# Kernel optimization log

Measured on AMD Instinct MI355X. Metric: run time of the kernel, lower is better.

Reference implementation:

```python
import jax, jax.numpy as jnp
import numpy as np

EMBED_DIM = 1024
NUM_HEADS = 16
HEAD_DIM = EMBED_DIM // NUM_HEADS
SCALE = HEAD_DIM ** -0.5


def setup_inputs() -> dict:
    key = jax.random.key(0)
    ks = jax.random.split(key, 9)
    B, N = 2, 2048
    s = EMBED_DIM ** -0.5  # ~ torch Linear init scale
    x = jax.random.normal(ks[0], (B, N, EMBED_DIM), dtype=jnp.float32)
    Wq = jax.random.uniform(ks[1], (EMBED_DIM, EMBED_DIM), jnp.float32, -s, s)
    bq = jax.random.uniform(ks[2], (EMBED_DIM,), jnp.float32, -s, s)
    Wk = jax.random.uniform(ks[3], (EMBED_DIM, EMBED_DIM), jnp.float32, -s, s)
    bk = jax.random.uniform(ks[4], (EMBED_DIM,), jnp.float32, -s, s)
    Wv = jax.random.uniform(ks[5], (EMBED_DIM, EMBED_DIM), jnp.float32, -s, s)
    bv = jax.random.uniform(ks[6], (EMBED_DIM,), jnp.float32, -s, s)
    Wo = jax.random.uniform(ks[7], (EMBED_DIM, EMBED_DIM), jnp.float32, -s, s)
    bo = jax.random.uniform(ks[8], (EMBED_DIM,), jnp.float32, -s, s)
    return {"x": x, "Wq": Wq, "bq": bq, "Wk": Wk, "bk": bk,
            "Wv": Wv, "bv": bv, "Wo": Wo, "bo": bo}


def reference(x, Wq, bq, Wk, bk, Wv, bv, Wo, bo):
    B, N, R = x.shape
    H, D = NUM_HEADS, HEAD_DIM
    # projections: Linear(x) = x @ W^T + b; reshape to (B, H, N, D)
    def proj(W, b):
        return (x @ W.T + b).reshape(B, N, H, D).transpose(0, 2, 1, 3)
    q = proj(Wq, bq)
    k = proj(Wk, bk)
    v = proj(Wv, bv)
    attn = jnp.einsum('bhnd,bhmd->bhnm', q, k) * SCALE  # (B,H,N,N)
    attn = jax.nn.softmax(attn, axis=-1)
    out = jnp.einsum('bhnm,bhmd->bhnd', attn, v)        # (B,H,N,D)
    out = out.transpose(0, 2, 1, 3).reshape(B, N, R)
    return out @ Wo.T + bo
```

## Files before the change

### kernel.cpp

```cpp
#include <hip/hip_runtime.h>
#include <stdint.h>

typedef __bf16 bf16;
typedef __bf16 bf16x4 __attribute__((ext_vector_type(4)));
typedef __bf16 bf16x8 __attribute__((ext_vector_type(8)));
typedef float f32x4 __attribute__((ext_vector_type(4)));

#define MFMA16(a, b, c) __builtin_amdgcn_mfma_f32_16x16x32_bf16((a), (b), (c), 0, 0, 0)

#define EMBED 1024
#define SEQ   2048
#define MROWS 4096
#define ATTN_SCALE 0.125f

__device__ __forceinline__ void gl2lds16(const bf16* g, bf16* l) {
    __builtin_amdgcn_global_load_lds(
        (const __attribute__((address_space(1))) void*)g,
        (__attribute__((address_space(3))) void*)l,
        16, 0, 0);
}

__global__ __launch_bounds__(256) void cast_all_kernel(
    const float* __restrict__ x,  const float* __restrict__ Wq,
    const float* __restrict__ Wk, const float* __restrict__ Wv,
    const float* __restrict__ Wo, bf16* __restrict__ dst) {
    const int blk = blockIdx.x;
    const float* src;
    size_t so, dofs;
    if (blk < 2048) {
        src = x; so = (size_t)blk * 2048; dofs = so;
    } else {
        const int w = (blk - 2048) >> 9;
        so  = (size_t)((blk - 2048) & 511) * 2048;
        src = (w == 0) ? Wq : (w == 1) ? Wk : (w == 2) ? Wv : Wo;
        dofs = (size_t)(4 + w) * 1024 * 1024 + so;
    }
    const size_t i = (size_t)threadIdx.x * 8;
    float4 a = *(const float4*)(src + so + i);
    float4 b = *(const float4*)(src + so + i + 4);
    bf16x8 o;
    o[0] = (bf16)a.x; o[1] = (bf16)a.y; o[2] = (bf16)a.z; o[3] = (bf16)a.w;
    o[4] = (bf16)b.x; o[5] = (bf16)b.y; o[6] = (bf16)b.z; o[7] = (bf16)b.w;
    *(bf16x8*)(dst + dofs + i) = o;
}

template <bool SCALE>
__device__ __forceinline__ void gemm_tile(const bf16* __restrict__ A,
                                          const bf16* __restrict__ W,
                                          const float* __restrict__ bias,
                                          bf16* __restrict__ C,
                                          int m0, int n0, bf16* smem) {
    bf16* As = smem;
    bf16* Bs = smem + 128 * 64;

    const int lane = threadIdx.x & 63;
    const int wv   = threadIdx.x >> 6;
    const int wm   = (wv >> 1) * 64;
    const int wn   = (wv & 1) * 64;
    const int fr   = lane & 15;
    const int quad = lane >> 4;
    const int srow = wv * 8 + (lane >> 3);
    const int swz  = (((lane & 7) ^ ((lane >> 3) & 7))) * 8;

    f32x4 acc[4][4];
#pragma unroll
    for (int mt = 0; mt < 4; ++mt)
#pragma unroll
        for (int nt = 0; nt < 4; ++nt)
            acc[mt][nt] = (f32x4){0.f, 0.f, 0.f, 0.f};

    for (int k0 = 0; k0 < 1024; k0 += 64) {
#pragma unroll
        for (int i = 0; i < 4; ++i) {
            gl2lds16(A + (size_t)(m0 + i * 32 + srow) * 1024 + k0 + swz,
                     &As[(i * 32 + wv * 8) * 64]);
            gl2lds16(W + (size_t)(n0 + i * 32 + srow) * 1024 + k0 + swz,
                     &Bs[(i * 32 + wv * 8) * 64]);
        }
        __syncthreads();
#pragma unroll
        for (int ks = 0; ks < 2; ++ks) {
            const int fcol = ((ks * 4 + quad) ^ (fr & 7)) * 8;
            bf16x8 af[4], bfr[4];
#pragma unroll
            for (int t = 0; t < 4; ++t) {
                af[t]  = *(const bf16x8*)&As[(wm + t * 16 + fr) * 64 + fcol];
                bfr[t] = *(const bf16x8*)&Bs[(wn + t * 16 + fr) * 64 + fcol];
            }
#pragma unroll
            for (int mt = 0; mt < 4; ++mt)
#pragma unroll
                for (int nt = 0; nt < 4; ++nt)
                    acc[mt][nt] = MFMA16(af[mt], bfr[nt], acc[mt][nt]);
        }
        __syncthreads();
    }

    float bv[4];
#pragma unroll
    for (int nt = 0; nt < 4; ++nt)
        bv[nt] = bias[n0 + wn + nt * 16 + fr];
    const int row4 = quad * 4;
#pragma unroll
    for (int mt = 0; mt < 4; ++mt)
#pragma unroll
        for (int nt = 0; nt < 4; ++nt)
#pragma unroll
            for (int r = 0; r < 4; ++r) {
                int m = m0 + wm + mt * 16 + row4 + r;
                int n = n0 + wn + nt * 16 + fr;
                float v = acc[mt][nt][r] + bv[nt];
                if (SCALE) v *= ATTN_SCALE;
                C[(size_t)m * 1024 + n] = (bf16)v;
            }
}

__device__ __forceinline__ void v_tile(const bf16* __restrict__ x,
                                       const bf16* __restrict__ Wv,
                                       const float* __restrict__ bias,
                                       bf16* __restrict__ VT,
                                       int m0, int n0, bf16* smem) {
    bf16* As = smem;
    bf16* Bs = smem + 128 * 64;

    const int lane = threadIdx.x & 63;
    const int wv   = threadIdx.x >> 6;
    const int wmW  = (wv >> 1) * 64;
    const int wnT  = (wv & 1) * 64;
    const int f    = lane & 15;
    const int quad = lane >> 4;
    const int srow = wv * 8 + (lane >> 3);
    const int swz  = (((lane & 7) ^ ((lane >> 3) & 7))) * 8;

    f32x4 acc[4][4];
#pragma unroll
    for (int mt = 0; mt < 4; ++mt)
#pragma unroll
        for (int nt = 0; nt < 4; ++nt)
            acc[mt][nt] = (f32x4){0.f, 0.f, 0.f, 0.f};

    for (int k0 = 0; k0 < 1024; k0 += 64) {
#pragma unroll
        for (int i = 0; i < 4; ++i) {
            gl2lds16(x  + (size_t)(m0 + i * 32 + srow) * 1024 + k0 + swz,
                     &As[(i * 32 + wv * 8) * 64]);
            gl2lds16(Wv + (size_t)(n0 + i * 32 + srow) * 1024 + k0 + swz,
                     &Bs[(i * 32 + wv * 8) * 64]);
        }
        __syncthreads();
#pragma unroll
        for (int ks = 0; ks < 2; ++ks) {
            const int fcol = ((ks * 4 + quad) ^ (f & 7)) * 8;
            bf16x8 wf[4], xf[4];
#pragma unroll
            for (int t = 0; t < 4; ++t) {
                wf[t] = *(const bf16x8*)&Bs[(wmW + t * 16 + f) * 64 + fcol];
                xf[t] = *(const bf16x8*)&As[(wnT + t * 16 + f) * 64 + fcol];
            }
#pragma unroll
            for (int mt = 0; mt < 4; ++mt)
#pragma unroll
                for (int nt = 0; nt < 4; ++nt)
                    acc[mt][nt] = MFMA16(wf[mt], xf[nt], acc[mt][nt]);
        }
        __syncthreads();
    }

    float4 b4[4];
#pragma unroll
    for (int mt = 0; mt < 4; ++mt)
        b4[mt] = *(const float4*)&bias[n0 + wmW + mt * 16 + quad * 4];

#pragma unroll
    for (int mt = 0; mt < 4; ++mt)
#pragma unroll
        for (int nt = 0; nt < 4; ++nt) {
            const int tok = wnT + nt * 16 + f;
#pragma unroll
            for (int r = 0; r < 4; ++r) {
                const float bvr = (r == 0) ? b4[mt].x : (r == 1) ? b4[mt].y
                                : (r == 2) ? b4[mt].z : b4[mt].w;
                smem[(wmW + mt * 16 + quad * 4 + r) * 136 + tok] =
                    (bf16)(acc[mt][nt][r] + bvr);
            }
        }
    __syncthreads();

    const int n_r  = threadIdx.x >> 4;
    const int t8   = (threadIdx.x & 15) * 8;
    const int base = t8 & ~31;
    const int u4   = ((t8 >> 3) & 3) * 4;
    const int bb   = m0 >> 11;
    const int tokg = (m0 & 2047) + t8;
#pragma unroll
    for (int p = 0; p < 8; ++p) {
        const int n_loc = p * 16 + n_r;
        const bf16* row = &smem[n_loc * 136];
        bf16x4 a = *(const bf16x4*)&row[base + u4];
        bf16x4 b = *(const bf16x4*)&row[base + 16 + u4];
        bf16x8 v = {a[0], a[1], a[2], a[3], b[0], b[1], b[2], b[3]};
        *(bf16x8*)&VT[((size_t)(bb * 1024 + n0 + n_loc)) * 2048 + tokg] = v;
    }
}

__global__ __launch_bounds__(256) void qkv_kernel(
    const bf16* __restrict__ x,
    const bf16* __restrict__ Wq, const float* __restrict__ bq,
    const bf16* __restrict__ Wk, const float* __restrict__ bk,
    const bf16* __restrict__ Wv, const float* __restrict__ bv,
    bf16* __restrict__ Q, bf16* __restrict__ K, bf16* __restrict__ VT) {
    __shared__ __align__(16) bf16 smem[128 * 136];
    const int m0    = blockIdx.x * 128;
    const int which = blockIdx.y >> 3;
    const int n0    = (blockIdx.y & 7) * 128;
    if (which == 0)      gemm_tile<true>(x, Wq, bq, Q, m0, n0, smem);
    else if (which == 1) gemm_tile<false>(x, Wk, bk, K, m0, n0, smem);
    else                 v_tile(x, Wv, bv, VT, m0, n0, smem);
}

__global__ __launch_bounds__(256) void oproj_kernel(
    const bf16* __restrict__ A, const bf16* __restrict__ W,
    const float* __restrict__ bias, float* __restrict__ C) {
    const int m0 = blockIdx.x * 128;
    const int n0 = blockIdx.y * 64;

    __shared__ bf16 As[128 * 64];
    __shared__ bf16 Bs[64 * 64];

    const int lane = threadIdx.x & 63;
    const int wv   = threadIdx.x >> 6;
    const int wm   = (wv >> 1) * 64;
    const int wn   = (wv & 1) * 32;
    const int fr   = lane & 15;
    const int quad = lane >> 4;
    const int srow = wv * 8 + (lane >> 3);
    const int swz  = (((lane & 7) ^ ((lane >> 3) & 7))) * 8;

    f32x4 acc[4][2];
#pragma unroll
    for (int mt = 0; mt < 4; ++mt)
#pragma unroll
        for (int nt = 0; nt < 2; ++nt)
            acc[mt][nt] = (f32x4){0.f, 0.f, 0.f, 0.f};

    for (int k0 = 0; k0 < 1024; k0 += 64) {
#pragma unroll
        for (int i = 0; i < 4; ++i)
            gl2lds16(A + (size_t)(m0 + i * 32 + srow) * 1024 + k0 + swz,
                     &As[(i * 32 + wv * 8) * 64]);
#pragma unroll
        for (int i = 0; i < 2; ++i)
            gl2lds16(W + (size_t)(n0 + i * 32 + srow) * 1024 + k0 + swz,
                     &Bs[(i * 32 + wv * 8) * 64]);
        __syncthreads();
#pragma unroll
        for (int ks = 0; ks < 2; ++ks) {
            const int fcol = ((ks * 4 + quad) ^ (fr & 7)) * 8;
            bf16x8 af[4], bfr[2];
#pragma unroll
            for (int t = 0; t < 4; ++t)
                af[t] = *(const bf16x8*)&As[(wm + t * 16 + fr) * 64 + fcol];
#pragma unroll
            for (int t = 0; t < 2; ++t)
                bfr[t] = *(const bf16x8*)&Bs[(wn + t * 16 + fr) * 64 + fcol];
#pragma unroll
            for (int mt = 0; mt < 4; ++mt)
#pragma unroll
                for (int nt = 0; nt < 2; ++nt)
                    acc[mt][nt] = MFMA16(af[mt], bfr[nt], acc[mt][nt]);
        }
        __syncthreads();
    }

    float bv[2];
#pragma unroll
    for (int nt = 0; nt < 2; ++nt)
        bv[nt] = bias[n0 + wn + nt * 16 + fr];
    const int row4 = quad * 4;
#pragma unroll
    for (int mt = 0; mt < 4; ++mt)
#pragma unroll
        for (int nt = 0; nt < 2; ++nt)
#pragma unroll
            for (int r = 0; r < 4; ++r) {
                int m = m0 + wm + mt * 16 + row4 + r;
                int n = n0 + wn + nt * 16 + fr;
                C[(size_t)m * 1024 + n] = acc[mt][nt][r] + bv[nt];
            }
}

__global__ __launch_bounds__(256, 2) void attn_kernel(
    const bf16* __restrict__ Q, const bf16* __restrict__ K,
    const bf16* __restrict__ VT, bf16* __restrict__ Opart,
    float* __restrict__ lpart) {
    const int tid  = threadIdx.x;
    const int lane = tid & 63;
    const int wv   = tid >> 6;
    const int quad = lane >> 4;
    const int f    = lane & 15;
    const int qt   = blockIdx.x >> 1;
    const int half = blockIdx.x & 1;
    const int q0   = qt * 256;
    const int kvb  = half * 1024;
    const int b    = blockIdx.y >> 4;
    const int h    = blockIdx.y & 15;

    const bf16* Qp = Q + ((size_t)b * SEQ) * 1024 + (size_t)h * 64;
    const bf16* Kp = K + ((size_t)b * SEQ) * 1024 + (size_t)h * 64;
    const bf16* Vp = VT + ((size_t)(b * 1024 + h * 64)) * 2048;
    bf16*  Op = Opart + (size_t)half * MROWS * 1024
                      + ((size_t)b * SEQ) * 1024 + (size_t)h * 64;
    float* lp = lpart + ((size_t)(half * 2 + b) * 16 + h) * SEQ;

    __shared__ bf16 Ks[2][64 * 64];
    __shared__ bf16 VTs[2][64 * 64];

    bf16x8 qf[4][2];
#pragma unroll
    for (int qg = 0; qg < 4; ++qg) {
        const bf16* qrow = Qp + (size_t)(q0 + wv * 64 + qg * 16 + f) * 1024;
        qf[qg][0] = *(const bf16x8*)(qrow + quad * 8);
        qf[qg][1] = *(const bf16x8*)(qrow + 32 + quad * 8);
    }

    const int srow = wv * 8 + (lane >> 3);
    const int swz  = (((lane & 7) ^ ((lane >> 3) & 7))) * 8;
    auto stageK = [&](int kv0, int buf) {
#pragma unroll
        for (int i = 0; i < 2; ++i)
            gl2lds16(Kp + (size_t)(kv0 + i * 32 + srow) * 1024 + swz,
                     &Ks[buf][(i * 32 + wv * 8) * 64]);
    };
    auto stageVT = [&](int kv0, int buf) {
#pragma unroll
        for (int i = 0; i < 2; ++i)
            gl2lds16(Vp + (size_t)(i * 32 + srow) * 2048 + kv0 + swz,
                     &VTs[buf][(i * 32 + wv * 8) * 64]);
    };

    stageK(kvb, 0);
    stageVT(kvb, 0);

    f32x4 oacc[4][4];
#pragma unroll
    for (int qg = 0; qg < 4; ++qg)
#pragma unroll
        for (int t = 0; t < 4; ++t)
            oacc[qg][t] = (f32x4){0.f, 0.f, 0.f, 0.f};
    f32x4 lacc[4];
#pragma unroll
    for (int qg = 0; qg < 4; ++qg)
        lacc[qg] = (f32x4){0.f, 0.f, 0.f, 0.f};
    const bf16x8 ones8 = {(bf16)1.f, (bf16)1.f, (bf16)1.f, (bf16)1.f,
                          (bf16)1.f, (bf16)1.f, (bf16)1.f, (bf16)1.f};
    const f32x4  zero4 = (f32x4){0.f, 0.f, 0.f, 0.f};

    const int fcol0 = (quad ^ (f & 7)) * 8;
    const int fcol1 = ((4 + quad) ^ (f & 7)) * 8;

    __syncthreads();

    auto step = [&](int cur, int nextit) {
        if (nextit < 16) {
            stageK(kvb + nextit * 64, cur ^ 1);
            stageVT(kvb + nextit * 64, cur ^ 1);
        }

        bf16x8 kf0[4], kf1[4];
#pragma unroll
        for (int t = 0; t < 4; ++t) {
            kf0[t] = *(const bf16x8*)&Ks[cur][(t * 16 + f) * 64 + fcol0];
            kf1[t] = *(const bf16x8*)&Ks[cur][(t * 16 + f) * 64 + fcol1];
        }
        bf16x8 pb8[4][2];
#pragma unroll
        for (int qg = 0; qg < 4; ++qg) {
            f32x4 s[4];
#pragma unroll
            for (int t = 0; t < 4; ++t) {
                s[t] = MFMA16(kf0[t], qf[qg][0], zero4);
                s[t] = MFMA16(kf1[t], qf[qg][1], s[t]);
            }
#pragma unroll
            for (int kt = 0; kt < 2; ++kt) {
#pragma unroll
                for (int r = 0; r < 4; ++r) {
                    pb8[qg][kt][r]     = (bf16)__expf(s[2 * kt][r]);
                    pb8[qg][kt][4 + r] = (bf16)__expf(s[2 * kt + 1][r]);
                }
                lacc[qg] = MFMA16(ones8, pb8[qg][kt], lacc[qg]);
            }
        }

#pragma unroll
        for (int dt = 0; dt < 4; ++dt) {
#pragma unroll
            for (int kt = 0; kt < 2; ++kt) {
                const int pc = ((kt * 4 + quad) ^ (f & 7)) * 8;
                bf16x8 vf = *(const bf16x8*)&VTs[cur][(dt * 16 + f) * 64 + pc];
#pragma unroll
                for (int qg = 0; qg < 4; ++qg)
                    oacc[qg][dt] = MFMA16(vf, pb8[qg][kt], oacc[qg][dt]);
            }
        }
        __syncthreads();
    };

    for (int it = 0; it < 16; it += 2) {
        step(0, it + 1);
        step(1, it + 2);
    }

#pragma unroll
    for (int qg = 0; qg < 4; ++qg) {
        const int q = q0 + wv * 64 + qg * 16 + f;
        bf16* orow = Op + (size_t)q * 1024;
#pragma unroll
        for (int dt = 0; dt < 4; ++dt) {
            bf16x4 ov;
#pragma unroll
            for (int r = 0; r < 4; ++r)
                ov[r] = (bf16)oacc[qg][dt][r];
            *(bf16x4*)(orow + dt * 16 + quad * 4) = ov;
        }
        if (quad == 0)
            lp[q] = lacc[qg][0];
    }
}

__global__ __launch_bounds__(256) void combine_kernel(
    const bf16* __restrict__ Opart, const float* __restrict__ lpart,
    bf16* __restrict__ O) {
    const int gid = blockIdx.x * 256 + threadIdx.x;
    const int row = gid >> 7;
    const int c8  = (gid & 127) * 8;
    const int b   = row >> 11;
    const int tok = row & 2047;
    const int h   = c8 >> 6;

    const float l = lpart[((size_t)(0 * 2 + b) * 16 + h) * SEQ + tok]
                  + lpart[((size_t)(1 * 2 + b) * 16 + h) * SEQ + tok];
    const float inv = 1.0f / l;

    const size_t off = (size_t)row * 1024 + c8;
    bf16x8 a = *(const bf16x8*)&Opart[off];
    bf16x8 c = *(const bf16x8*)&Opart[(size_t)MROWS * 1024 + off];
    bf16x8 o;
#pragma unroll
    for (int i = 0; i < 8; ++i)
        o[i] = (bf16)(((float)a[i] + (float)c[i]) * inv);
    *(bf16x8*)&O[off] = o;
}

extern "C" void kernel_launch(void* const* d_in, const int* in_sizes, int n_in,
                              void* d_out, int out_size, void* d_ws, size_t ws_size,
                              hipStream_t stream) {
    const float* x  = (const float*)d_in[0];
    const float* Wq = (const float*)d_in[1];
    const float* bq = (const float*)d_in[2];
    const float* Wk = (const float*)d_in[3];
    const float* bk = (const float*)d_in[4];
    const float* Wv = (const float*)d_in[5];
    const float* bv = (const float*)d_in[6];
    const float* Wo = (const float*)d_in[7];
    const float* bo = (const float*)d_in[8];
    float* out = (float*)d_out;

    bf16* xb    = (bf16*)d_ws;
    bf16* Wqb   = xb   + (size_t)MROWS * 1024;
    bf16* Wkb   = Wqb  + (size_t)1024 * 1024;
    bf16* Wvb   = Wkb  + (size_t)1024 * 1024;
    bf16* Wob   = Wvb  + (size_t)1024 * 1024;
    bf16* Q     = Wob  + (size_t)1024 * 1024;
    bf16* K     = Q    + (size_t)MROWS * 1024;
    bf16* VT    = K    + (size_t)MROWS * 1024;
    bf16* O     = VT   + (size_t)MROWS * 1024;
    bf16* Opart = O    + (size_t)MROWS * 1024;
    float* lpart = (float*)(Opart + (size_t)2 * MROWS * 1024);

    cast_all_kernel<<<4096, 256, 0, stream>>>(x, Wq, Wk, Wv, Wo, xb);

    qkv_kernel<<<dim3(32, 24), 256, 0, stream>>>(xb, Wqb, bq, Wkb, bk, Wvb, bv, Q, K, VT);
    attn_kernel<<<dim3(16, 32), 256, 0, stream>>>(Q, K, VT, Opart, lpart);
    combine_kernel<<<2048, 256, 0, stream>>>(Opart, lpart, O);
    oproj_kernel<<<dim3(32, 16), 256, 0, stream>>>(O, Wob, bo, out);
}
```

Measured before the change: 193.6 us.

## Double-buffer GEMM tiles, deepen attention K/V prefetch, use exp2 with folded scale

The three GEMM paths (QKV projection, V-transpose tile, output projection) now stage the next K-tile into a second LDS buffer while computing the current one, with one barrier per iteration instead of two. The attention kernel moves from a 2-buffer to a 4-buffer ring with prefetch distance 2 and partial vmcnt waits, so loads stay in flight across barriers. The softmax exponent now uses native exp2, with log2(e) folded into the Q scale constant. MFMA sections are wrapped in s_setprio to favour matrix issue. LDS use roughly doubles, which may reduce occupancy.

```diff
diff --git a/kernel.cpp b/kernel.cpp
--- a/kernel.cpp
+++ b/kernel.cpp
@@ -11,7 +11,7 @@
 #define EMBED 1024
 #define SEQ   2048
 #define MROWS 4096
-#define ATTN_SCALE 0.125f
+#define ATTN_QSCALE 0.1803368801111f
 
 __device__ __forceinline__ void gl2lds16(const bf16* g, bf16* l) {
     __builtin_amdgcn_global_load_lds(
@@ -50,9 +50,6 @@
                                           const float* __restrict__ bias,
                                           bf16* __restrict__ C,
                                           int m0, int n0, bf16* smem) {
-    bf16* As = smem;
-    bf16* Bs = smem + 128 * 64;
-
     const int lane = threadIdx.x & 63;
     const int wv   = threadIdx.x >> 6;
     const int wm   = (wv >> 1) * 64;
@@ -69,7 +66,10 @@
         for (int nt = 0; nt < 4; ++nt)
             acc[mt][nt] = (f32x4){0.f, 0.f, 0.f, 0.f};
 
-    for (int k0 = 0; k0 < 1024; k0 += 64) {
+    auto stage = [&](int kt, int bb) {
+        bf16* As = smem + bb * 16384;
+        bf16* Bs = As + 8192;
+        const int k0 = kt * 64;
 #pragma unroll
         for (int i = 0; i < 4; ++i) {
             gl2lds16(A + (size_t)(m0 + i * 32 + srow) * 1024 + k0 + swz,
@@ -77,7 +77,17 @@
             gl2lds16(W + (size_t)(n0 + i * 32 + srow) * 1024 + k0 + swz,
                      &Bs[(i * 32 + wv * 8) * 64]);
         }
-        __syncthreads();
+    };
+
+    stage(0, 0);
+#pragma unroll
+    for (int kt = 0; kt < 16; ++kt) {
+        const int bb = kt & 1;
+        asm volatile("s_waitcnt vmcnt(0)" ::: "memory");
+        __builtin_amdgcn_s_barrier();
+        if (kt < 15) stage(kt + 1, bb ^ 1);
+        const bf16* As = smem + bb * 16384;
+        const bf16* Bs = As + 8192;
 #pragma unroll
         for (int ks = 0; ks < 2; ++ks) {
             const int fcol = ((ks * 4 + quad) ^ (fr & 7)) * 8;
@@ -87,13 +97,14 @@
                 af[t]  = *(const bf16x8*)&As[(wm + t * 16 + fr) * 64 + fcol];
                 bfr[t] = *(const bf16x8*)&Bs[(wn + t * 16 + fr) * 64 + fcol];
             }
+            __builtin_amdgcn_s_setprio(1);
 #pragma unroll
             for (int mt = 0; mt < 4; ++mt)
 #pragma unroll
                 for (int nt = 0; nt < 4; ++nt)
                     acc[mt][nt] = MFMA16(af[mt], bfr[nt], acc[mt][nt]);
-        }
-        __syncthreads();
+            __builtin_amdgcn_s_setprio(0);
+        }
     }
 
     float bv[4];
@@ -110,7 +121,7 @@
                 int m = m0 + wm + mt * 16 + row4 + r;
                 int n = n0 + wn + nt * 16 + fr;
                 float v = acc[mt][nt][r] + bv[nt];
-                if (SCALE) v *= ATTN_SCALE;
+                if (SCALE) v *= ATTN_QSCALE;
                 C[(size_t)m * 1024 + n] = (bf16)v;
             }
 }
@@ -120,9 +131,6 @@
                                        const float* __restrict__ bias,
                                        bf16* __restrict__ VT,
                                        int m0, int n0, bf16* smem) {
-    bf16* As = smem;
-    bf16* Bs = smem + 128 * 64;
-
     const int lane = threadIdx.x & 63;
     const int wv   = threadIdx.x >> 6;
     const int wmW  = (wv >> 1) * 64;
@@ -139,7 +147,10 @@
         for (int nt = 0; nt < 4; ++nt)
             acc[mt][nt] = (f32x4){0.f, 0.f, 0.f, 0.f};
 
-    for (int k0 = 0; k0 < 1024; k0 += 64) {
+    auto stage = [&](int kt, int bb) {
+        bf16* As = smem + bb * 16384;
+        bf16* Bs = As + 8192;
+        const int k0 = kt * 64;
 #pragma unroll
         for (int i = 0; i < 4; ++i) {
             gl2lds16(x  + (size_t)(m0 + i * 32 + srow) * 1024 + k0 + swz,
@@ -147,7 +158,17 @@
             gl2lds16(Wv + (size_t)(n0 + i * 32 + srow) * 1024 + k0 + swz,
                      &Bs[(i * 32 + wv * 8) * 64]);
         }
-        __syncthreads();
+    };
+
+    stage(0, 0);
+#pragma unroll
+    for (int kt = 0; kt < 16; ++kt) {
+        const int bb = kt & 1;
+        asm volatile("s_waitcnt vmcnt(0)" ::: "memory");
+        __builtin_amdgcn_s_barrier();
+        if (kt < 15) stage(kt + 1, bb ^ 1);
+        const bf16* As = smem + bb * 16384;
+        const bf16* Bs = As + 8192;
 #pragma unroll
         for (int ks = 0; ks < 2; ++ks) {
             const int fcol = ((ks * 4 + quad) ^ (f & 7)) * 8;
@@ -157,19 +178,22 @@
                 wf[t] = *(const bf16x8*)&Bs[(wmW + t * 16 + f) * 64 + fcol];
                 xf[t] = *(const bf16x8*)&As[(wnT + t * 16 + f) * 64 + fcol];
             }
+            __builtin_amdgcn_s_setprio(1);
 #pragma unroll
             for (int mt = 0; mt < 4; ++mt)
 #pragma unroll
                 for (int nt = 0; nt < 4; ++nt)
                     acc[mt][nt] = MFMA16(wf[mt], xf[nt], acc[mt][nt]);
-        }
-        __syncthreads();
+            __builtin_amdgcn_s_setprio(0);
+        }
     }
 
     float4 b4[4];
 #pragma unroll
     for (int mt = 0; mt < 4; ++mt)
         b4[mt] = *(const float4*)&bias[n0 + wmW + mt * 16 + quad * 4];
+
+    __syncthreads();
 
 #pragma unroll
     for (int mt = 0; mt < 4; ++mt)
@@ -209,7 +233,7 @@
     const bf16* __restrict__ Wk, const float* __restrict__ bk,
     const bf16* __restrict__ Wv, const float* __restrict__ bv,
     bf16* __restrict__ Q, bf16* __restrict__ K, bf16* __restrict__ VT) {
-    __shared__ __align__(16) bf16 smem[128 * 136];
+    __shared__ __align__(16) bf16 smem[32768];
     const int m0    = blockIdx.x * 128;
     const int which = blockIdx.y >> 3;
     const int n0    = (blockIdx.y & 7) * 128;
@@ -224,8 +248,7 @@
     const int m0 = blockIdx.x * 128;
     const int n0 = blockIdx.y * 64;
 
-    __shared__ bf16 As[128 * 64];
-    __shared__ bf16 Bs[64 * 64];
+    __shared__ __align__(16) bf16 smem[24576];
 
     const int lane = threadIdx.x & 63;
     const int wv   = threadIdx.x >> 6;
@@ -243,7 +266,10 @@
         for (int nt = 0; nt < 2; ++nt)
             acc[mt][nt] = (f32x4){0.f, 0.f, 0.f, 0.f};
 
-    for (int k0 = 0; k0 < 1024; k0 += 64) {
+    auto stage = [&](int kt, int bb) {
+        bf16* As = smem + bb * 12288;
+        bf16* Bs = As + 8192;
+        const int k0 = kt * 64;
 #pragma unroll
         for (int i = 0; i < 4; ++i)
             gl2lds16(A + (size_t)(m0 + i * 32 + srow) * 1024 + k0 + swz,
@@ -252,7 +278,17 @@
         for (int i = 0; i < 2; ++i)
             gl2lds16(W + (size_t)(n0 + i * 32 + srow) * 1024 + k0 + swz,
                      &Bs[(i * 32 + wv * 8) * 64]);
-        __syncthreads();
+    };
+
+    stage(0, 0);
+#pragma unroll
+    for (int kt = 0; kt < 16; ++kt) {
+        const int bb = kt & 1;
+        asm volatile("s_waitcnt vmcnt(0)" ::: "memory");
+        __builtin_amdgcn_s_barrier();
+        if (kt < 15) stage(kt + 1, bb ^ 1);
+        const bf16* As = smem + bb * 12288;
+        const bf16* Bs = As + 8192;
 #pragma unroll
         for (int ks = 0; ks < 2; ++ks) {
             const int fcol = ((ks * 4 + quad) ^ (fr & 7)) * 8;
@@ -263,13 +299,14 @@
 #pragma unroll
             for (int t = 0; t < 2; ++t)
                 bfr[t] = *(const bf16x8*)&Bs[(wn + t * 16 + fr) * 64 + fcol];
+            __builtin_amdgcn_s_setprio(1);
 #pragma unroll
             for (int mt = 0; mt < 4; ++mt)
 #pragma unroll
                 for (int nt = 0; nt < 2; ++nt)
                     acc[mt][nt] = MFMA16(af[mt], bfr[nt], acc[mt][nt]);
-        }
-        __syncthreads();
+            __builtin_amdgcn_s_setprio(0);
+        }
     }
 
     float bv[2];
@@ -312,8 +349,8 @@
                       + ((size_t)b * SEQ) * 1024 + (size_t)h * 64;
     float* lp = lpart + ((size_t)(half * 2 + b) * 16 + h) * SEQ;
 
-    __shared__ bf16 Ks[2][64 * 64];
-    __shared__ bf16 VTs[2][64 * 64];
+    __shared__ bf16 Ks[4][64 * 64];
+    __shared__ bf16 VTs[4][64 * 64];
 
     bf16x8 qf[4][2];
 #pragma unroll
@@ -325,21 +362,23 @@
 
     const int srow = wv * 8 + (lane >> 3);
     const int swz  = (((lane & 7) ^ ((lane >> 3) & 7))) * 8;
-    auto stageK = [&](int kv0, int buf) {
+    auto stageK = [&](int t, int bb) {
+        const int kv0 = kvb + t * 64;
 #pragma unroll
         for (int i = 0; i < 2; ++i)
             gl2lds16(Kp + (size_t)(kv0 + i * 32 + srow) * 1024 + swz,
-                     &Ks[buf][(i * 32 + wv * 8) * 64]);
+                     &Ks[bb][(i * 32 + wv * 8) * 64]);
     };
-    auto stageVT = [&](int kv0, int buf) {
+    auto stageVT = [&](int t, int bb) {
+        const int kv0 = kvb + t * 64;
 #pragma unroll
         for (int i = 0; i < 2; ++i)
             gl2lds16(Vp + (size_t)(i * 32 + srow) * 2048 + kv0 + swz,
-                     &VTs[buf][(i * 32 + wv * 8) * 64]);
+                     &VTs[bb][(i * 32 + wv * 8) * 64]);
     };
 
-    stageK(kvb, 0);
-    stageVT(kvb, 0);
+    stageK(0, 0); stageVT(0, 0);
+    stageK(1, 1); stageVT(1, 1);
 
     f32x4 oacc[4][4];
 #pragma unroll
@@ -358,58 +397,60 @@
     const int fcol0 = (quad ^ (f & 7)) * 8;
     const int fcol1 = ((4 + quad) ^ (f & 7)) * 8;
 
-    __syncthreads();
-
-    auto step = [&](int cur, int nextit) {
-        if (nextit < 16) {
-            stageK(kvb + nextit * 64, cur ^ 1);
-            stageVT(kvb + nextit * 64, cur ^ 1);
-        }
+    auto step = [&](int t, int bb, int drain) {
+        if (drain == 8) { stageK(t + 2, (t + 2) & 3); stageVT(t + 2, (t + 2) & 3); }
+        if (drain == 8)      asm volatile("s_waitcnt vmcnt(8)" ::: "memory");
+        else if (drain == 4) asm volatile("s_waitcnt vmcnt(4)" ::: "memory");
+        else                 asm volatile("s_waitcnt vmcnt(0)" ::: "memory");
+        __builtin_amdgcn_s_barrier();
 
         bf16x8 kf0[4], kf1[4];
 #pragma unroll
-        for (int t = 0; t < 4; ++t) {
-            kf0[t] = *(const bf16x8*)&Ks[cur][(t * 16 + f) * 64 + fcol0];
-            kf1[t] = *(const bf16x8*)&Ks[cur][(t * 16 + f) * 64 + fcol1];
+        for (int t4 = 0; t4 < 4; ++t4) {
+            kf0[t4] = *(const bf16x8*)&Ks[bb][(t4 * 16 + f) * 64 + fcol0];
+            kf1[t4] = *(const bf16x8*)&Ks[bb][(t4 * 16 + f) * 64 + fcol1];
         }
         bf16x8 pb8[4][2];
 #pragma unroll
         for (int qg = 0; qg < 4; ++qg) {
             f32x4 s[4];
-#pragma unroll
-            for (int t = 0; t < 4; ++t) {
-                s[t] = MFMA16(kf0[t], qf[qg][0], zero4);
-                s[t] = MFMA16(kf1[t], qf[qg][1], s[t]);
-            }
+            __builtin_amdgcn_s_setprio(1);
+#pragma unroll
+            for (int t4 = 0; t4 < 4; ++t4) {
+                s[t4] = MFMA16(kf0[t4], qf[qg][0], zero4);
+                s[t4] = MFMA16(kf1[t4], qf[qg][1], s[t4]);
+            }
+            __builtin_amdgcn_s_setprio(0);
 #pragma unroll
             for (int kt = 0; kt < 2; ++kt) {
 #pragma unroll
                 for (int r = 0; r < 4; ++r) {
-                    pb8[qg][kt][r]     = (bf16)__expf(s[2 * kt][r]);
-                    pb8[qg][kt][4 + r] = (bf16)__expf(s[2 * kt + 1][r]);
+                    pb8[qg][kt][r]     = (bf16)__builtin_amdgcn_exp2f(s[2 * kt][r]);
+                    pb8[qg][kt][4 + r] = (bf16)__builtin_amdgcn_exp2f(s[2 * kt + 1][r]);
                 }
                 lacc[qg] = MFMA16(ones8, pb8[qg][kt], lacc[qg]);
             }
         }
 
+        __builtin_amdgcn_s_setprio(1);
 #pragma unroll
         for (int dt = 0; dt < 4; ++dt) {
 #pragma unroll
             for (int kt = 0; kt < 2; ++kt) {
                 const int pc = ((kt * 4 + quad) ^ (f & 7)) * 8;
-                bf16x8 vf = *(const bf16x8*)&VTs[cur][(dt * 16 + f) * 64 + pc];
+                bf16x8 vf = *(const bf16x8*)&VTs[bb][(dt * 16 + f) * 64 + pc];
 #pragma unroll
                 for (int qg = 0; qg < 4; ++qg)
                     oacc[qg][dt] = MFMA16(vf, pb8[qg][kt], oacc[qg][dt]);
             }
         }
-        __syncthreads();
+        __builtin_amdgcn_s_setprio(0);
     };
 
-    for (int it = 0; it < 16; it += 2) {
-        step(0, it + 1);
-        step(1, it + 2);
-    }
+    for (int tt = 0; tt < 12; tt += 4) {
+        step(tt, 0, 8); step(tt + 1, 1, 8); step(tt + 2, 2, 8); step(tt + 3, 3, 8);
+    }
+    step(12, 0, 8); step(13, 1, 8); step(14, 2, 4); step(15, 3, 0);
 
 #pragma unroll
     for (int qg = 0; qg < 4; ++qg) {
```

Measured after the change: 179.9 us. -7.0%, faster.
